# Optimization experiments

Hardware: AMD Instinct MI355X
Metric: run time of the kernel (lower is better)

The kernel has to match this reference:

```python
import jax, jax.numpy as jnp
import numpy as np
import math

BATCH, SEQ, D_MODEL, HEADS = 2, 2048, 1024, 16
DK = D_MODEL // HEADS  # 64
THETA = 10000.0


def _init_linear(key, d_in, d_out):
    std = math.sqrt(2.0 / (d_in + d_out))
    return (jax.random.truncated_normal(key, -3.0, 3.0, (d_in, d_out), jnp.float32) * std)


def setup_inputs() -> dict:
    key = jax.random.key(0)
    kx, kq, kk, kv, ko = jax.random.split(key, 5)
    x = jax.random.normal(kx, (BATCH, SEQ, D_MODEL), jnp.float32)
    W_Q = _init_linear(kq, D_MODEL, D_MODEL)
    W_K = _init_linear(kk, D_MODEL, D_MODEL)
    W_V = _init_linear(kv, D_MODEL, D_MODEL)
    W_O = _init_linear(ko, D_MODEL, D_MODEL)
    token_positions = jnp.arange(SEQ, dtype=jnp.int64 if jax.config.jax_enable_x64 else jnp.int32)
    # RoPE tables: angle[i, k] = i / theta**(2k/d_k), shape [max_seq_len, d_k//2]
    pos = jnp.arange(SEQ, dtype=jnp.float32)[:, None]
    inv_freq = THETA ** (-2.0 * jnp.arange(DK // 2, dtype=jnp.float32) / DK)
    angles = pos * inv_freq
    return {
        "x": x,
        "token_positions": token_positions,
        "W_Q": W_Q,
        "W_K": W_K,
        "W_V": W_V,
        "W_O": W_O,
        "cos": jnp.cos(angles),
        "sin": jnp.sin(angles),
    }


def _apply_rope(t, cos_p, sin_p):
    # t: [B, H, S, DK]; cos_p/sin_p: [S, DK//2] (already gathered by position)
    t_even = t[..., 0::2]
    t_odd = t[..., 1::2]
    even_rot = cos_p * t_even - sin_p * t_odd
    odd_rot = sin_p * t_even + cos_p * t_odd
    # interleave back: [..., DK//2, 2] -> [..., DK]
    return jnp.stack([even_rot, odd_rot], axis=-1).reshape(t.shape)


def reference(x, token_positions, W_Q, W_K, W_V, W_O, cos, sin):
    B, S, D = x.shape
    H, dk = HEADS, D // HEADS
    # QKV projections, split into heads: [B, S, D] -> [B, H, S, dk]
    def proj(W):
        return jnp.einsum("bsd,de->bse", x, W).reshape(B, S, H, dk).transpose(0, 2, 1, 3)
    Q, K, V = proj(W_Q), proj(W_K), proj(W_V)
    cos_p = cos[token_positions]  # [S, dk//2]
    sin_p = sin[token_positions]
    Q = _apply_rope(Q, cos_p, sin_p)
    K = _apply_rope(K, cos_p, sin_p)
    scores = jnp.einsum("bhqd,bhkd->bhqk", Q, K) / jnp.sqrt(jnp.asarray(dk, x.dtype))
    causal = jnp.tril(jnp.ones((S, S), dtype=bool))
    scores = jnp.where(causal, scores, -jnp.inf)
    attn = jax.nn.softmax(scores, axis=-1)
    out = jnp.einsum("bhqk,bhkd->bhqd", attn, V)  # [B, H, S, dk]
    out = out.transpose(0, 2, 1, 3).reshape(B, S, D)
    return jnp.einsum("bsd,de->bse", out, W_O)
```

## Files before the change

kernel.cpp:

```cpp
#include <hip/hip_runtime.h>

typedef unsigned short u16;
typedef unsigned int   u32;
typedef __bf16  bf16x8 __attribute__((ext_vector_type(8)));
typedef float   f32x4  __attribute__((ext_vector_type(4)));
typedef u32     u32x4  __attribute__((ext_vector_type(4)));

#define SEQ    2048
#define HEADS  16
#define DM     1024
#define NBH    32
#define NBS    4096

#define LOG2E  1.4426950408889634f

__device__ __forceinline__ u16 f2b(float f) {
    u32 x;
    __builtin_memcpy(&x, &f, 4);
    return (u16)((x + 0x7fffu + ((x >> 16) & 1u)) >> 16);
}

__device__ __forceinline__ u32 pkc(float lo, float hi) {
    __bf16 a = (__bf16)lo, b = (__bf16)hi;
    u16 x, y;
    __builtin_memcpy(&x, &a, 2);
    __builtin_memcpy(&y, &b, 2);
    return (u32)x | ((u32)y << 16);
}

__device__ __forceinline__ bf16x8 ld_bf8(const u16* p) {
    return *(const bf16x8*)p;
}

__device__ __forceinline__ void gl_lds16(const u16* g, __bf16* l) {
    __builtin_amdgcn_global_load_lds(
        (__attribute__((address_space(1))) void*)g,
        (__attribute__((address_space(3))) void*)l,
        16, 0, 0);
}

__global__ __launch_bounds__(256) void transpose_wqkv(const float* __restrict__ Wq,
                                                      const float* __restrict__ Wk,
                                                      const float* __restrict__ Wv,
                                                      u16* __restrict__ WqkvT) {
    __shared__ u16 tile[64][65];
    const int z  = blockIdx.z;
    const float* src = (z == 0) ? Wq : (z == 1) ? Wk : Wv;
    const int k0 = blockIdx.x * 64, n0 = blockIdx.y * 64;
    const int tid = threadIdx.x;
    for (int i = 0; i < 16; ++i) {
        int e = i * 256 + tid;
        int r = e >> 6, c = e & 63;
        tile[r][c] = f2b(src[(size_t)(k0 + r) * DM + n0 + c]);
    }
    __syncthreads();
    u16* dst = WqkvT + (size_t)z * DM * DM;
    for (int i = 0; i < 16; ++i) {
        int e = i * 256 + tid;
        int r = e >> 6, c = e & 63;
        dst[(size_t)(n0 + r) * DM + k0 + c] = tile[c][r];
    }
}

__global__ __launch_bounds__(256) void transpose_wo(const float* __restrict__ Wo,
                                                    u16* __restrict__ WoT) {
    __shared__ u16 tile[64][65];
    const int k0 = blockIdx.x * 64, n0 = blockIdx.y * 64;
    const int tid = threadIdx.x;
    for (int i = 0; i < 16; ++i) {
        int e = i * 256 + tid;
        int r = e >> 6, c = e & 63;
        tile[r][c] = f2b(Wo[(size_t)(k0 + r) * DM + n0 + c]);
    }
    __syncthreads();
    for (int i = 0; i < 16; ++i) {
        int e = i * 256 + tid;
        int r = e >> 6, c = e & 63;
        WoT[(size_t)(n0 + r) * DM + k0 + c] = tile[c][r];
    }
}

__global__ __launch_bounds__(256) void cvt_x(const float* __restrict__ x,
                                             u16* __restrict__ xb) {
    int t = blockIdx.x * 256 + threadIdx.x;
    const float* p = x + (size_t)t * 8;
    f32x4 a = *(const f32x4*)p;
    f32x4 b = *(const f32x4*)(p + 4);
    u32x4 v;
    v[0] = pkc(a[0], a[1]);
    v[1] = pkc(a[2], a[3]);
    v[2] = pkc(b[0], b[1]);
    v[3] = pkc(b[2], b[3]);
    *(u32x4*)(xb + (size_t)t * 8) = v;
}

__global__ __launch_bounds__(256) void gemm_qkv(const u16* __restrict__ Ab,
                                                const u16* __restrict__ Bt,
                                                u16* __restrict__ Qp,
                                                u16* __restrict__ Kp,
                                                u16* __restrict__ Vt,
                                                const float* __restrict__ cosT,
                                                const float* __restrict__ sinT) {
    __shared__ __attribute__((aligned(16))) __bf16 As[128 * 64];
    __shared__ __attribute__((aligned(16))) __bf16 Bs[128 * 64];
    const int tid  = threadIdx.x;
    const int wave = tid >> 6, lane = tid & 63;
    const int quad = lane >> 4, col = lane & 15;
    const int wm = wave >> 1, wn = wave & 1;
    const int m0 = blockIdx.x * 128, n0 = blockIdx.y * 128;
    const int srow = tid >> 3;
    const int aslot = (((tid & 7) ^ (srow & 7)) << 3);
    const int c7 = col & 7;

    f32x4 zero = {0.f, 0.f, 0.f, 0.f};
    f32x4 acc[4][4];
    for (int i = 0; i < 4; ++i)
        for (int j = 0; j < 4; ++j) acc[i][j] = zero;

    for (int k0 = 0; k0 < DM; k0 += 64) {
        __syncthreads();
#pragma unroll
        for (int p = 0; p < 4; ++p)
            gl_lds16(Ab + (size_t)(m0 + p * 32 + srow) * DM + k0 + aslot,
                     &As[p * 2048 + tid * 8]);
#pragma unroll
        for (int p = 0; p < 4; ++p)
            gl_lds16(Bt + (size_t)(n0 + p * 32 + srow) * DM + k0 + aslot,
                     &Bs[p * 2048 + tid * 8]);
        __syncthreads();
#pragma unroll
        for (int ks = 0; ks < 2; ++ks) {
            const int rsl = ((((ks << 2) | quad) ^ c7) << 3);
            bf16x8 af[4], bfr[4];
#pragma unroll
            for (int mt = 0; mt < 4; ++mt)
                af[mt] = *(const bf16x8*)&As[(wm * 64 + mt * 16 + col) * 64 + rsl];
#pragma unroll
            for (int nt = 0; nt < 4; ++nt)
                bfr[nt] = *(const bf16x8*)&Bs[(wn * 64 + nt * 16 + col) * 64 + rsl];
#pragma unroll
            for (int mt = 0; mt < 4; ++mt)
#pragma unroll
                for (int nt = 0; nt < 4; ++nt)
                    acc[mt][nt] = __builtin_amdgcn_mfma_f32_16x16x32_bf16(
                        af[mt], bfr[nt], acc[mt][nt], 0, 0, 0);
        }
    }

    const int which = blockIdx.y >> 3;
    if (which < 2) {
        u16* dst = (which == 0) ? Qp : Kp;
        const float sc = (which == 0) ? 0.125f * LOG2E : 1.f;
        for (int mt = 0; mt < 4; ++mt)
            for (int nt = 0; nt < 4; ++nt) {
                const int d = nt * 16 + col;
                const int p = d >> 1;
                const int h = ((n0 + wn * 64 + nt * 16 + col) & 1023) >> 6;
                for (int r = 0; r < 4; ++r) {
                    int row = m0 + wm * 64 + mt * 16 + quad * 4 + r;
                    int s = row & (SEQ - 1);
                    int bb = row >> 11;
                    float c  = cosT[s * 32 + p];
                    float sn = sinT[s * 32 + p];
                    float self = acc[mt][nt][r];
                    float part = __shfl_xor(self, 1);
                    float out = (col & 1) ? (sn * part + c * self)
                                          : (c * self - sn * part);
                    out *= sc;
                    dst[(((size_t)(bb * HEADS + h)) * SEQ + s) * 64 + d] = f2b(out);
                }
            }
    } else {
        for (int mt = 0; mt < 4; ++mt)
            for (int nt = 0; nt < 4; ++nt) {
                int c1 = (n0 + wn * 64 + nt * 16 + col) & 1023;
                int h = c1 >> 6, d = c1 & 63;
                for (int r = 0; r < 4; ++r) {
                    int row = m0 + wm * 64 + mt * 16 + quad * 4 + r;
                    int bb = row >> 11, s = row & (SEQ - 1);
                    Vt[(((size_t)(bb * HEADS + h)) * 64 + d) * SEQ + s] =
                        f2b(acc[mt][nt][r]);
                }
            }
    }
}

__global__ __launch_bounds__(256) void gemm_wo(const u16* __restrict__ A,
                                               const u16* __restrict__ Bt,
                                               float* __restrict__ C) {
    __shared__ __attribute__((aligned(16))) __bf16 As[128 * 64];
    __shared__ __attribute__((aligned(16))) __bf16 Bs[64 * 64];
    const int tid  = threadIdx.x;
    const int wave = tid >> 6, lane = tid & 63;
    const int quad = lane >> 4, col = lane & 15;
    const int m0 = blockIdx.x * 128, n0 = blockIdx.y * 64;
    const int srow = tid >> 3;
    const int aslot = (((tid & 7) ^ (srow & 7)) << 3);
    const int c7 = col & 7;

    f32x4 zero = {0.f, 0.f, 0.f, 0.f};
    f32x4 acc[2][4];
    for (int i = 0; i < 2; ++i)
        for (int j = 0; j < 4; ++j) acc[i][j] = zero;

    for (int k0 = 0; k0 < DM; k0 += 64) {
        __syncthreads();
#pragma unroll
        for (int p = 0; p < 4; ++p)
            gl_lds16(A + (size_t)(m0 + p * 32 + srow) * DM + k0 + aslot,
                     &As[p * 2048 + tid * 8]);
#pragma unroll
        for (int p = 0; p < 2; ++p)
            gl_lds16(Bt + (size_t)(n0 + p * 32 + srow) * DM + k0 + aslot,
                     &Bs[p * 2048 + tid * 8]);
        __syncthreads();
#pragma unroll
        for (int ks = 0; ks < 2; ++ks) {
            const int rsl = ((((ks << 2) | quad) ^ c7) << 3);
            bf16x8 af[2], bfr[4];
#pragma unroll
            for (int mt = 0; mt < 2; ++mt)
                af[mt] = *(const bf16x8*)&As[(wave * 32 + mt * 16 + col) * 64 + rsl];
#pragma unroll
            for (int nt = 0; nt < 4; ++nt)
                bfr[nt] = *(const bf16x8*)&Bs[(nt * 16 + col) * 64 + rsl];
#pragma unroll
            for (int mt = 0; mt < 2; ++mt)
#pragma unroll
                for (int nt = 0; nt < 4; ++nt)
                    acc[mt][nt] = __builtin_amdgcn_mfma_f32_16x16x32_bf16(
                        af[mt], bfr[nt], acc[mt][nt], 0, 0, 0);
        }
    }

    for (int mt = 0; mt < 2; ++mt)
        for (int nt = 0; nt < 4; ++nt)
            for (int r = 0; r < 4; ++r) {
                int row = m0 + wave * 32 + mt * 16 + quad * 4 + r;
                int cc  = n0 + nt * 16 + col;
                C[(size_t)row * DM + cc] = acc[mt][nt][r];
            }
}

__global__ __launch_bounds__(256, 3) void flash_attn(const u16* __restrict__ Qp,
                                                     const u16* __restrict__ Kp,
                                                     const u16* __restrict__ Vt,
                                                     u16* __restrict__ O) {
    __shared__ float os[4][32][68];
    __shared__ float mM[4][32];
    __shared__ float mL[4][32];
    const int tid  = threadIdx.x;
    const int wave = tid >> 6, lane = tid & 63;
    const int quad = lane >> 4, col = lane & 15;
    const bool hi5 = lane >= 32;
    const bool hi4 = (lane & 16) != 0;
    const int bh = blockIdx.x;
    const int b = bh >> 4, h = bh & 15;
    const int qt = 63 - blockIdx.y;
    const int q0 = qt * 32;

    const u16* Qb = Qp + (size_t)bh * SEQ * 64;
    const u16* Kb = Kp + (size_t)bh * SEQ * 64;
    const u16* Vb = Vt + (size_t)bh * 64 * SEQ;

    bf16x8 bq00 = ld_bf8(Qb + (size_t)(q0 + col) * 64 + quad * 8);
    bf16x8 bq01 = ld_bf8(Qb + (size_t)(q0 + col) * 64 + 32 + quad * 8);
    bf16x8 bq10 = ld_bf8(Qb + (size_t)(q0 + 16 + col) * 64 + quad * 8);
    bf16x8 bq11 = ld_bf8(Qb + (size_t)(q0 + 16 + col) * 64 + 32 + quad * 8);

    f32x4 zero = {0.f, 0.f, 0.f, 0.f};
    f32x4 o0[4] = {zero, zero, zero, zero};
    f32x4 o1[4] = {zero, zero, zero, zero};
    float m0_ = -1e30f, m1_ = -1e30f;
    float lp0 = 0.f, lp1 = 0.f;

    const int nkt = qt + 1;
    int kt = wave;
    bf16x8 ck00, ck01, ck10, ck11, cv0, cv1, cv2, cv3;
    if (kt < nkt) {
        const int kb = kt << 5;
        ck00 = ld_bf8(Kb + (size_t)(kb + col) * 64 + quad * 8);
        ck01 = ld_bf8(Kb + (size_t)(kb + col) * 64 + 32 + quad * 8);
        ck10 = ld_bf8(Kb + (size_t)(kb + 16 + col) * 64 + quad * 8);
        ck11 = ld_bf8(Kb + (size_t)(kb + 16 + col) * 64 + 32 + quad * 8);
        cv0  = ld_bf8(Vb + (size_t)(0 * 16 + col) * SEQ + kb + quad * 8);
        cv1  = ld_bf8(Vb + (size_t)(1 * 16 + col) * SEQ + kb + quad * 8);
        cv2  = ld_bf8(Vb + (size_t)(2 * 16 + col) * SEQ + kb + quad * 8);
        cv3  = ld_bf8(Vb + (size_t)(3 * 16 + col) * SEQ + kb + quad * 8);
    }

    for (; kt < nkt; kt += 4) {
        int kn = kt + 4; if (kn >= nkt) kn = kt;
        const int kb2 = kn << 5;
        bf16x8 nk00 = ld_bf8(Kb + (size_t)(kb2 + col) * 64 + quad * 8);
        bf16x8 nk01 = ld_bf8(Kb + (size_t)(kb2 + col) * 64 + 32 + quad * 8);
        bf16x8 nk10 = ld_bf8(Kb + (size_t)(kb2 + 16 + col) * 64 + quad * 8);
        bf16x8 nk11 = ld_bf8(Kb + (size_t)(kb2 + 16 + col) * 64 + 32 + quad * 8);
        bf16x8 nv0  = ld_bf8(Vb + (size_t)(0 * 16 + col) * SEQ + kb2 + quad * 8);
        bf16x8 nv1  = ld_bf8(Vb + (size_t)(1 * 16 + col) * SEQ + kb2 + quad * 8);
        bf16x8 nv2  = ld_bf8(Vb + (size_t)(2 * 16 + col) * SEQ + kb2 + quad * 8);
        bf16x8 nv3  = ld_bf8(Vb + (size_t)(3 * 16 + col) * SEQ + kb2 + quad * 8);

        f32x4 s00 = zero, s01 = zero, s10 = zero, s11 = zero;
        s00 = __builtin_amdgcn_mfma_f32_16x16x32_bf16(ck00, bq00, s00, 0, 0, 0);
        s10 = __builtin_amdgcn_mfma_f32_16x16x32_bf16(ck00, bq10, s10, 0, 0, 0);
        s00 = __builtin_amdgcn_mfma_f32_16x16x32_bf16(ck01, bq01, s00, 0, 0, 0);
        s10 = __builtin_amdgcn_mfma_f32_16x16x32_bf16(ck01, bq11, s10, 0, 0, 0);
        s01 = __builtin_amdgcn_mfma_f32_16x16x32_bf16(ck10, bq00, s01, 0, 0, 0);
        s11 = __builtin_amdgcn_mfma_f32_16x16x32_bf16(ck10, bq10, s11, 0, 0, 0);
        s01 = __builtin_amdgcn_mfma_f32_16x16x32_bf16(ck11, bq01, s01, 0, 0, 0);
        s11 = __builtin_amdgcn_mfma_f32_16x16x32_bf16(ck11, bq11, s11, 0, 0, 0);

        float v00[4], v01[4], v10[4], v11[4];
        float lm0 = -1e30f, lm1 = -1e30f;
        if (kt == qt) {
            for (int r = 0; r < 4; ++r) {
                int krel = quad * 4 + r;
                float a0 = (krel > col) ? -1e30f : s00[r];
                float b0 = -1e30f;
                float a1 = s10[r];
                float b1 = (krel > col) ? -1e30f : s11[r];
                v00[r] = a0; v01[r] = b0; v10[r] = a1; v11[r] = b1;
                lm0 = fmaxf(lm0, fmaxf(a0, b0));
                lm1 = fmaxf(lm1, fmaxf(a1, b1));
            }
        } else {
            for (int r = 0; r < 4; ++r) {
                v00[r] = s00[r]; v01[r] = s01[r];
                v10[r] = s10[r]; v11[r] = s11[r];
                lm0 = fmaxf(lm0, fmaxf(v00[r], v01[r]));
                lm1 = fmaxf(lm1, fmaxf(v10[r], v11[r]));
            }
        }

        float dd = fmaxf(lm0 - m0_, lm1 - m1_);
        if (__any(dd > 11.54f)) {
            float lr0 = fmaxf(lm0, __shfl_xor(lm0, 16));
            lr0 = fmaxf(lr0, __shfl_xor(lr0, 32));
            float lr1 = fmaxf(lm1, __shfl_xor(lm1, 16));
            lr1 = fmaxf(lr1, __shfl_xor(lr1, 32));
            float mn0 = fmaxf(m0_, lr0), mn1 = fmaxf(m1_, lr1);
            float al0 = __builtin_amdgcn_exp2f(m0_ - mn0);
            float al1 = __builtin_amdgcn_exp2f(m1_ - mn1);
            m0_ = mn0; m1_ = mn1;
            lp0 *= al0; lp1 *= al1;
            for (int r = 0; r < 4; ++r) {
                float ar0 = __shfl(al0, quad * 4 + r);
                float ar1 = __shfl(al1, quad * 4 + r);
                for (int nt = 0; nt < 4; ++nt) {
                    o0[nt][r] *= ar0;
                    o1[nt][r] *= ar1;
                }
            }
        }

        for (int r = 0; r < 4; ++r) {
            v00[r] = __builtin_amdgcn_exp2f(v00[r] - m0_);
            v01[r] = __builtin_amdgcn_exp2f(v01[r] - m0_);
            v10[r] = __builtin_amdgcn_exp2f(v10[r] - m1_);
            v11[r] = __builtin_amdgcn_exp2f(v11[r] - m1_);
            lp0 += v00[r] + v01[r];
            lp1 += v10[r] + v11[r];
        }

        u32 fwa0[4], fwa1[4];
        {
            u32 A0 = pkc(v00[0], v00[1]), A1 = pkc(v00[2], v00[3]);
            u32 B0 = pkc(v01[0], v01[1]), B1 = pkc(v01[2], v01[3]);
            u32 g0 = hi5 ? A0 : B0,  g1 = hi5 ? A1 : B1;
            u32 r0 = __shfl_xor(g0, 32), r1 = __shfl_xor(g1, 32);
            u32 P00 = hi5 ? r0 : A0,  P01 = hi5 ? r1 : A1;
            u32 P10 = hi5 ? B0 : r0,  P11 = hi5 ? B1 : r1;
            u32 h0 = hi4 ? P00 : P10, h1 = hi4 ? P01 : P11;
            u32 u0 = __shfl_xor(h0, 16), u1 = __shfl_xor(h1, 16);
            fwa0[0] = hi4 ? u0 : P00;  fwa0[1] = hi4 ? u1 : P01;
            fwa0[2] = hi4 ? P10 : u0;  fwa0[3] = hi4 ? P11 : u1;
        }
        {
            u32 A0 = pkc(v10[0], v10[1]), A1 = pkc(v10[2], v10[3]);
            u32 B0 = pkc(v11[0], v11[1]), B1 = pkc(v11[2], v11[3]);
            u32 g0 = hi5 ? A0 : B0,  g1 = hi5 ? A1 : B1;
            u32 r0 = __shfl_xor(g0, 32), r1 = __shfl_xor(g1, 32);
            u32 P00 = hi5 ? r0 : A0,  P01 = hi5 ? r1 : A1;
            u32 P10 = hi5 ? B0 : r0,  P11 = hi5 ? B1 : r1;
            u32 h0 = hi4 ? P00 : P10, h1 = hi4 ? P01 : P11;
            u32 u0 = __shfl_xor(h0, 16), u1 = __shfl_xor(h1, 16);
            fwa1[0] = hi4 ? u0 : P00;  fwa1[1] = hi4 ? u1 : P01;
            fwa1[2] = hi4 ? P10 : u0;  fwa1[3] = hi4 ? P11 : u1;
        }
        bf16x8 pf0, pf1;
        __builtin_memcpy(&pf0, fwa0, 16);
        __builtin_memcpy(&pf1, fwa1, 16);

        o0[0] = __builtin_amdgcn_mfma_f32_16x16x32_bf16(pf0, cv0, o0[0], 0, 0, 0);
        o1[0] = __builtin_amdgcn_mfma_f32_16x16x32_bf16(pf1, cv0, o1[0], 0, 0, 0);
        o0[1] = __builtin_amdgcn_mfma_f32_16x16x32_bf16(pf0, cv1, o0[1], 0, 0, 0);
        o1[1] = __builtin_amdgcn_mfma_f32_16x16x32_bf16(pf1, cv1, o1[1], 0, 0, 0);
        o0[2] = __builtin_amdgcn_mfma_f32_16x16x32_bf16(pf0, cv2, o0[2], 0, 0, 0);
        o1[2] = __builtin_amdgcn_mfma_f32_16x16x32_bf16(pf1, cv2, o1[2], 0, 0, 0);
        o0[3] = __builtin_amdgcn_mfma_f32_16x16x32_bf16(pf0, cv3, o0[3], 0, 0, 0);
        o1[3] = __builtin_amdgcn_mfma_f32_16x16x32_bf16(pf1, cv3, o1[3], 0, 0, 0);

        ck00 = nk00; ck01 = nk01; ck10 = nk10; ck11 = nk11;
        cv0 = nv0; cv1 = nv1; cv2 = nv2; cv3 = nv3;
    }

    float lt0 = lp0;
    lt0 += __shfl_xor(lt0, 16); lt0 += __shfl_xor(lt0, 32);
    float lt1 = lp1;
    lt1 += __shfl_xor(lt1, 16); lt1 += __shfl_xor(lt1, 32);
    if (quad == 0) {
        mM[wave][col] = m0_;      mL[wave][col] = lt0;
        mM[wave][16 + col] = m1_; mL[wave][16 + col] = lt1;
    }
    for (int nt = 0; nt < 4; ++nt)
        for (int r = 0; r < 4; ++r) {
            os[wave][quad * 4 + r][nt * 16 + col]      = o0[nt][r];
            os[wave][16 + quad * 4 + r][nt * 16 + col] = o1[nt][r];
        }
    __syncthreads();

    {
        const int q  = tid >> 3;
        const int d0 = (tid & 7) * 8;
        float M = fmaxf(fmaxf(mM[0][q], mM[1][q]), fmaxf(mM[2][q], mM[3][q]));
        float L = 0.f;
        f32x4 a0 = {0.f, 0.f, 0.f, 0.f}, a1 = {0.f, 0.f, 0.f, 0.f};
        for (int w = 0; w < 4; ++w) {
            float e = __builtin_amdgcn_exp2f(mM[w][q] - M);
            L += e * mL[w][q];
            f32x4 p0 = *(const f32x4*)&os[w][q][d0];
            f32x4 p1 = *(const f32x4*)&os[w][q][d0 + 4];
            for (int j = 0; j < 4; ++j) { a0[j] += e * p0[j]; a1[j] += e * p1[j]; }
        }
        float inv = 1.f / L;
        u32x4 val;
        val[0] = pkc(a0[0] * inv, a0[1] * inv);
        val[1] = pkc(a0[2] * inv, a0[3] * inv);
        val[2] = pkc(a1[0] * inv, a1[1] * inv);
        val[3] = pkc(a1[2] * inv, a1[3] * inv);
        *(u32x4*)&O[((size_t)b * SEQ + q0 + q) * DM + h * 64 + d0] = val;
    }
}

extern "C" void kernel_launch(void* const* d_in, const int* in_sizes, int n_in,
                              void* d_out, int out_size, void* d_ws, size_t ws_size,
                              hipStream_t stream) {
    const float* x    = (const float*)d_in[0];
    const float* Wq   = (const float*)d_in[2];
    const float* Wk   = (const float*)d_in[3];
    const float* Wv   = (const float*)d_in[4];
    const float* Wo   = (const float*)d_in[5];
    const float* cosT = (const float*)d_in[6];
    const float* sinT = (const float*)d_in[7];
    float* out = (float*)d_out;

    u16* ws    = (u16*)d_ws;
    u16* qp    = ws;
    u16* kp    = ws + 4194304;
    u16* vt    = ws + 8388608;
    u16* woT   = ws + 8388608;
    u16* wqkvT = ws + 12582912;
    u16* ao    = ws + 12582912;
    u16* xb    = (u16*)out;

    dim3 blk(256);
    transpose_wqkv<<<dim3(16, 16, 3), blk, 0, stream>>>(Wq, Wk, Wv, wqkvT);
    cvt_x<<<dim3(2048), blk, 0, stream>>>(x, xb);
    gemm_qkv<<<dim3(32, 24), blk, 0, stream>>>(xb, wqkvT, qp, kp, vt, cosT, sinT);
    flash_attn<<<dim3(NBH, 64), blk, 0, stream>>>(qp, kp, vt, ao);
    transpose_wo<<<dim3(16, 16), blk, 0, stream>>>(Wo, woT);
    gemm_wo<<<dim3(32, 16), blk, 0, stream>>>(ao, woT, out);
}
```

Before: 224.0 us.

## Use permlane swaps for P relayout and shrink attention merge LDS

```diff
diff --git a/kernel.cpp b/kernel.cpp
--- a/kernel.cpp
+++ b/kernel.cpp
@@ -30,6 +30,13 @@
 
 __device__ __forceinline__ bf16x8 ld_bf8(const u16* p) {
     return *(const bf16x8*)p;
+}
+
+__device__ __forceinline__ void pl32swap(u32 &a, u32 &b) {
+    asm volatile("v_permlane32_swap_b32 %0, %1" : "+v"(a), "+v"(b));
+}
+__device__ __forceinline__ void pl16swap(u32 &a, u32 &b) {
+    asm volatile("v_permlane16_swap_b32 %0, %1" : "+v"(a), "+v"(b));
 }
 
 __device__ __forceinline__ void gl_lds16(const u16* g, __bf16* l) {
@@ -242,18 +249,16 @@
             }
 }
 
-__global__ __launch_bounds__(256, 3) void flash_attn(const u16* __restrict__ Qp,
+__global__ __launch_bounds__(256, 6) void flash_attn(const u16* __restrict__ Qp,
                                                      const u16* __restrict__ Kp,
                                                      const u16* __restrict__ Vt,
                                                      u16* __restrict__ O) {
-    __shared__ float os[4][32][68];
-    __shared__ float mM[4][32];
-    __shared__ float mL[4][32];
+    __shared__ float osm[3][32][66];
+    __shared__ float mMm[3][32];
+    __shared__ float mLm[3][32];
     const int tid  = threadIdx.x;
     const int wave = tid >> 6, lane = tid & 63;
     const int quad = lane >> 4, col = lane & 15;
-    const bool hi5 = lane >= 32;
-    const bool hi4 = (lane & 16) != 0;
     const int bh = blockIdx.x;
     const int b = bh >> 4, h = bh & 15;
     const int qt = 63 - blockIdx.y;
@@ -363,34 +368,23 @@
             lp1 += v10[r] + v11[r];
         }
 
-        u32 fwa0[4], fwa1[4];
+        bf16x8 pf0, pf1;
         {
             u32 A0 = pkc(v00[0], v00[1]), A1 = pkc(v00[2], v00[3]);
             u32 B0 = pkc(v01[0], v01[1]), B1 = pkc(v01[2], v01[3]);
-            u32 g0 = hi5 ? A0 : B0,  g1 = hi5 ? A1 : B1;
-            u32 r0 = __shfl_xor(g0, 32), r1 = __shfl_xor(g1, 32);
-            u32 P00 = hi5 ? r0 : A0,  P01 = hi5 ? r1 : A1;
-            u32 P10 = hi5 ? B0 : r0,  P11 = hi5 ? B1 : r1;
-            u32 h0 = hi4 ? P00 : P10, h1 = hi4 ? P01 : P11;
-            u32 u0 = __shfl_xor(h0, 16), u1 = __shfl_xor(h1, 16);
-            fwa0[0] = hi4 ? u0 : P00;  fwa0[1] = hi4 ? u1 : P01;
-            fwa0[2] = hi4 ? P10 : u0;  fwa0[3] = hi4 ? P11 : u1;
+            pl32swap(A0, B0);  pl32swap(A1, B1);
+            pl16swap(A0, B0);  pl16swap(A1, B1);
+            u32 fwa[4] = {A0, A1, B0, B1};
+            __builtin_memcpy(&pf0, fwa, 16);
         }
         {
             u32 A0 = pkc(v10[0], v10[1]), A1 = pkc(v10[2], v10[3]);
             u32 B0 = pkc(v11[0], v11[1]), B1 = pkc(v11[2], v11[3]);
-            u32 g0 = hi5 ? A0 : B0,  g1 = hi5 ? A1 : B1;
-            u32 r0 = __shfl_xor(g0, 32), r1 = __shfl_xor(g1, 32);
-            u32 P00 = hi5 ? r0 : A0,  P01 = hi5 ? r1 : A1;
-            u32 P10 = hi5 ? B0 : r0,  P11 = hi5 ? B1 : r1;
-            u32 h0 = hi4 ? P00 : P10, h1 = hi4 ? P01 : P11;
-            u32 u0 = __shfl_xor(h0, 16), u1 = __shfl_xor(h1, 16);
-            fwa1[0] = hi4 ? u0 : P00;  fwa1[1] = hi4 ? u1 : P01;
-            fwa1[2] = hi4 ? P10 : u0;  fwa1[3] = hi4 ? P11 : u1;
-        }
-        bf16x8 pf0, pf1;
-        __builtin_memcpy(&pf0, fwa0, 16);
-        __builtin_memcpy(&pf1, fwa1, 16);
+            pl32swap(A0, B0);  pl32swap(A1, B1);
+            pl16swap(A0, B0);  pl16swap(A1, B1);
+            u32 fwa[4] = {A0, A1, B0, B1};
+            __builtin_memcpy(&pf1, fwa, 16);
+        }
 
         o0[0] = __builtin_amdgcn_mfma_f32_16x16x32_bf16(pf0, cv0, o0[0], 0, 0, 0);
         o1[0] = __builtin_amdgcn_mfma_f32_16x16x32_bf16(pf1, cv0, o1[0], 0, 0, 0);
@@ -409,37 +403,65 @@
     lt0 += __shfl_xor(lt0, 16); lt0 += __shfl_xor(lt0, 32);
     float lt1 = lp1;
     lt1 += __shfl_xor(lt1, 16); lt1 += __shfl_xor(lt1, 32);
-    if (quad == 0) {
-        mM[wave][col] = m0_;      mL[wave][col] = lt0;
-        mM[wave][16 + col] = m1_; mL[wave][16 + col] = lt1;
-    }
-    for (int nt = 0; nt < 4; ++nt)
+
+    if (wave > 0) {
+        const int w = wave - 1;
+        if (quad == 0) {
+            mMm[w][col] = m0_;       mLm[w][col] = lt0;
+            mMm[w][16 + col] = m1_;  mLm[w][16 + col] = lt1;
+        }
+        for (int nt = 0; nt < 4; ++nt)
+            for (int r = 0; r < 4; ++r) {
+                osm[w][quad * 4 + r][nt * 16 + col]      = o0[nt][r];
+                osm[w][16 + quad * 4 + r][nt * 16 + col] = o1[nt][r];
+            }
+    }
+    __syncthreads();
+
+    if (wave == 0) {
         for (int r = 0; r < 4; ++r) {
-            os[wave][quad * 4 + r][nt * 16 + col]      = o0[nt][r];
-            os[wave][16 + quad * 4 + r][nt * 16 + col] = o1[nt][r];
-        }
-    __syncthreads();
-
-    {
-        const int q  = tid >> 3;
-        const int d0 = (tid & 7) * 8;
-        float M = fmaxf(fmaxf(mM[0][q], mM[1][q]), fmaxf(mM[2][q], mM[3][q]));
-        float L = 0.f;
-        f32x4 a0 = {0.f, 0.f, 0.f, 0.f}, a1 = {0.f, 0.f, 0.f, 0.f};
-        for (int w = 0; w < 4; ++w) {
-            float e = __builtin_amdgcn_exp2f(mM[w][q] - M);
-            L += e * mL[w][q];
-            f32x4 p0 = *(const f32x4*)&os[w][q][d0];
-            f32x4 p1 = *(const f32x4*)&os[w][q][d0 + 4];
-            for (int j = 0; j < 4; ++j) { a0[j] += e * p0[j]; a1[j] += e * p1[j]; }
-        }
-        float inv = 1.f / L;
-        u32x4 val;
-        val[0] = pkc(a0[0] * inv, a0[1] * inv);
-        val[1] = pkc(a0[2] * inv, a0[3] * inv);
-        val[2] = pkc(a1[0] * inv, a1[1] * inv);
-        val[3] = pkc(a1[2] * inv, a1[3] * inv);
-        *(u32x4*)&O[((size_t)b * SEQ + q0 + q) * DM + h * 64 + d0] = val;
+            const int qr = quad * 4 + r;
+            {
+                float mw = __shfl(m0_, qr);
+                float lw = __shfl(lt0, qr);
+                float M = fmaxf(fmaxf(mw, mMm[0][qr]),
+                                fmaxf(mMm[1][qr], mMm[2][qr]));
+                float e0 = __builtin_amdgcn_exp2f(mw - M);
+                float e1 = __builtin_amdgcn_exp2f(mMm[0][qr] - M);
+                float e2 = __builtin_amdgcn_exp2f(mMm[1][qr] - M);
+                float e3 = __builtin_amdgcn_exp2f(mMm[2][qr] - M);
+                float L = e0 * lw + e1 * mLm[0][qr] + e2 * mLm[1][qr] +
+                          e3 * mLm[2][qr];
+                float inv = 1.f / L;
+                for (int nt = 0; nt < 4; ++nt) {
+                    int dd = nt * 16 + col;
+                    float a = e0 * o0[nt][r] + e1 * osm[0][qr][dd] +
+                              e2 * osm[1][qr][dd] + e3 * osm[2][qr][dd];
+                    O[((size_t)b * SEQ + q0 + qr) * DM + h * 64 + dd] =
+                        f2b(a * inv);
+                }
+            }
+            {
+                float mw = __shfl(m1_, qr);
+                float lw = __shfl(lt1, qr);
+                float M = fmaxf(fmaxf(mw, mMm[0][16 + qr]),
+                                fmaxf(mMm[1][16 + qr], mMm[2][16 + qr]));
+                float e0 = __builtin_amdgcn_exp2f(mw - M);
+                float e1 = __builtin_amdgcn_exp2f(mMm[0][16 + qr] - M);
+                float e2 = __builtin_amdgcn_exp2f(mMm[1][16 + qr] - M);
+                float e3 = __builtin_amdgcn_exp2f(mMm[2][16 + qr] - M);
+                float L = e0 * lw + e1 * mLm[0][16 + qr] +
+                          e2 * mLm[1][16 + qr] + e3 * mLm[2][16 + qr];
+                float inv = 1.f / L;
+                for (int nt = 0; nt < 4; ++nt) {
+                    int dd = nt * 16 + col;
+                    float a = e0 * o1[nt][r] + e1 * osm[0][16 + qr][dd] +
+                              e2 * osm[1][16 + qr][dd] + e3 * osm[2][16 + qr][dd];
+                    O[((size_t)b * SEQ + q0 + 16 + qr) * DM + h * 64 + dd] =
+                        f2b(a * inv);
+                }
+            }
+        }
     }
 }
 
```

After: 523.4 us. +133.6%, slower.
